# Kernel optimization log

Measured on AMD Instinct MI355X. Metric: run time of the kernel, lower is better.

Reference implementation:

```python
import jax, jax.numpy as jnp
import numpy as np

NUM_HEADS = 1


def setup_inputs() -> dict:
    key = jax.random.key(0)
    k1, k2, k3 = jax.random.split(key, 3)
    B, C, H, W = 32, 1024, 32, 32
    x = jax.random.normal(k1, (B, C, H, W), dtype=jnp.float32)
    w_qkv = jax.random.normal(k2, (3 * C, C), dtype=jnp.float32) * (C ** -0.5)
    w_proj = jax.random.normal(k3, (C, C), dtype=jnp.float32) * (C ** -0.5)
    b_proj = jnp.zeros((C,), dtype=jnp.float32)
    return {"x": x, "w_qkv": w_qkv, "w_proj": w_proj, "b_proj": b_proj}


def reference(x, w_qkv, w_proj, b_proj):
    B, C, H, W = x.shape
    nh = NUM_HEADS
    hd = C // nh
    S = H * W
    # 1x1 conv (no bias) == channel matmul
    qkv = jnp.einsum('bchw,oc->bohw', x, w_qkv)          # [B, 3C, H, W]
    qkv = qkv.reshape(B * nh, 3 * hd, S)
    q, k, v = jnp.split(qkv, 3, axis=1)                   # each [B*nh, hd, S]
    scale = hd ** -0.25
    attn = jax.nn.softmax(
        jnp.einsum('bct,bcs->bts', q * scale, k * scale), axis=-1)  # [B*nh, S, S]
    # faithful to source einsum 'bts,bcs->bts': sums v over channel dim only
    h = attn * jnp.sum(v, axis=1, keepdims=True)          # [B*nh, S, S]
    h = h.reshape(B, nh * S, H, W)                        # requires nh*S == C
    out = jnp.einsum('bchw,oc->bohw', h, w_proj) + b_proj[None, :, None, None]
    return out + x
```

## Files before the change

kernel.cpp:

```cpp
#include <hip/hip_runtime.h>
#include <hip/hip_bf16.h>
#include <stdint.h>


typedef __attribute__((ext_vector_type(8))) short short8;
typedef __attribute__((ext_vector_type(4))) float f32x4;

__device__ __forceinline__ short f2b(float f) {
    __hip_bfloat16 h = __float2bfloat16(f);
    return *reinterpret_cast<short*>(&h);
}
__device__ __forceinline__ float b2f(short s) {
    __hip_bfloat16 h;
    *reinterpret_cast<short*>(&h) = s;
    return __bfloat162float(h);
}

#define GLOAD16(gp, lp) __builtin_amdgcn_global_load_lds(                      \
    (const __attribute__((address_space(1))) unsigned int*)(gp),               \
    (__attribute__((address_space(3))) unsigned int*)(lp), 16, 0, 0)

#define WAITV4 asm volatile("s_waitcnt vmcnt(4)" ::: "memory")
#define WAITV0 asm volatile("s_waitcnt vmcnt(0)" ::: "memory")
#define WAITL0 asm volatile("s_waitcnt lgkmcnt(0)" ::: "memory")
#define BAR()  { asm volatile("" ::: "memory"); __builtin_amdgcn_s_barrier(); \
                 asm volatile("" ::: "memory"); }

__global__ void k_wvsum(const float* __restrict__ wqkv, float* __restrict__ wvsum) {
    int c = blockIdx.x * 256 + threadIdx.x;
    float s = 0.f;
    const float* p = wqkv + (size_t)2048 * 1024 + c;
    for (int o = 0; o < 1024; ++o) s += p[(size_t)o * 1024];
    wvsum[c] = s;
}

__global__ void k_cvt(const float* __restrict__ in, short* __restrict__ out) {
    int i = (blockIdx.x * 256 + threadIdx.x) * 4;
    #pragma unroll
    for (int j = 0; j < 4; ++j) out[i + j] = f2b(in[i + j]);
}

__global__ void k_xpose(const float* __restrict__ x, const float* __restrict__ wvsum,
                        short* __restrict__ xT, float* __restrict__ vsum) {
    __shared__ float tile[32][33];
    __shared__ float ps[8][32];
    int b = blockIdx.z;
    int s0 = blockIdx.x * 32, c0 = blockIdx.y * 32;
    int tx = threadIdx.x, ty = threadIdx.y;
    const float* xb = x + ((size_t)b << 20);
    float p = 0.f;
    #pragma unroll
    for (int i = 0; i < 4; ++i) {
        int cl = ty + i * 8;
        float v = xb[(size_t)(c0 + cl) * 1024 + s0 + tx];
        tile[cl][tx] = v;
        p += v * wvsum[c0 + cl];
    }
    ps[ty][tx] = p;
    __syncthreads();
    short* xTb = xT + ((size_t)b << 20);
    #pragma unroll
    for (int i = 0; i < 4; ++i) {
        int sl = ty + i * 8;
        xTb[(size_t)(s0 + sl) * 1024 + c0 + tx] = f2b(tile[tx][sl]);
    }
    if (ty == 0) {
        float s = 0.f;
        #pragma unroll
        for (int i = 0; i < 8; ++i) s += ps[i][tx];
        atomicAdd(&vsum[b * 1024 + s0 + tx], s);
    }
}

template <int MODE, int TM, int TN>
__global__ __launch_bounds__(512, 2)
void k_gemm(const short* __restrict__ A0, size_t strideA, int lda,
            const short* __restrict__ B0, size_t strideB, int ldb,
            void* __restrict__ O0, size_t strideO, int ldo,
            float* __restrict__ Z,
            const float* __restrict__ vsum,
            const float* __restrict__ bias,
            const float* __restrict__ xres) {
    __shared__ __align__(16) short As[2 * 256 * 64];
    __shared__ __align__(16) short Bs[2 * 256 * 64];

    constexpr int TPB = TM * TN;
    constexpr int CPX = TPB * 4;
    int wg = blockIdx.x;
    int swz = (wg & 7) * CPX + (wg >> 3);
    int z = swz / TPB;
    int rz = swz - z * TPB;
    int m0 = (rz / TN) * 256, n0 = (rz % TN) * 256;

    int tid = threadIdx.x;
    int wid = tid >> 6, l = tid & 63;
    int wm = wid >> 2, wn = wid & 3;
    int lr = l & 15, lg = l >> 4;

    const short* A = A0 + (size_t)z * strideA;
    const short* Bt = B0 + (size_t)z * strideB;

    int srow = wid * 16 + (l >> 3);
    int scol = ((l & 7) ^ (l >> 3)) * 8;
    const short* gA = A + (size_t)(m0 + srow) * lda + scol;
    const short* gB = Bt + (size_t)(n0 + srow) * ldb + scol;
    char* const ldsA = (char*)As;
    char* const ldsB = (char*)Bs;
    int sdst = wid * 2048;

    auto SA = [&](int buf, int h, int t) __attribute__((always_inline)) {
        const short* g = gA + (size_t)(h * 128) * lda + t * 64;
        char* d = ldsA + buf * 32768 + h * 16384 + sdst;
        GLOAD16(g, d);
        GLOAD16(g + (size_t)8 * lda, d + 1024);
    };
    auto SB = [&](int buf, int h, int t) __attribute__((always_inline)) {
        const short* g = gB + (size_t)(h * 128) * ldb + t * 64;
        char* d = ldsB + buf * 32768 + h * 16384 + sdst;
        GLOAD16(g, d);
        GLOAD16(g + (size_t)8 * ldb, d + 1024);
    };

    int cs0 = ((lg) ^ (lr & 7)) * 16;
    int cs1 = ((4 + lg) ^ (lr & 7)) * 16;
    int arow = (wm * 128 + lr) * 128;
    int brow = (wn * 64 + lr) * 128;

    short8 af[8], bf0[4], bf1[4];
    f32x4 acc[8][4] = {};

    auto LDA_ = [&](int buf, int mh) __attribute__((always_inline)) {
        const char* p = ldsA + buf * 32768 + arow + mh * 64 * 128;
        #pragma unroll
        for (int mi = 0; mi < 4; ++mi) {
            af[mi * 2]     = *(const short8*)(p + mi * 2048 + cs0);
            af[mi * 2 + 1] = *(const short8*)(p + mi * 2048 + cs1);
        }
    };
    auto LDB_ = [&](short8* dst, int buf, int nh) __attribute__((always_inline)) {
        const char* p = ldsB + buf * 32768 + brow + nh * 32 * 128;
        #pragma unroll
        for (int ni = 0; ni < 2; ++ni) {
            dst[ni * 2]     = *(const short8*)(p + ni * 2048 + cs0);
            dst[ni * 2 + 1] = *(const short8*)(p + ni * 2048 + cs1);
        }
    };
    auto MMA = [&](int mh, int nh, const short8* bfp) __attribute__((always_inline)) {
        __builtin_amdgcn_s_setprio(1);
        #pragma unroll
        for (int ks = 0; ks < 2; ++ks)
            #pragma unroll
            for (int mi = 0; mi < 4; ++mi)
                #pragma unroll
                for (int ni = 0; ni < 2; ++ni)
                    acc[mh * 4 + mi][nh * 2 + ni] =
                        __builtin_amdgcn_mfma_f32_16x16x32_bf16(
                            af[mi * 2 + ks], bfp[ni * 2 + ks],
                            acc[mh * 4 + mi][nh * 2 + ni], 0, 0, 0);
        __builtin_amdgcn_s_setprio(0);
    };

    SB(0, 0, 0); SB(0, 1, 0); SA(0, 0, 0); SA(0, 1, 0);
    SB(1, 0, 1); SB(1, 1, 1);
    WAITV4;
    BAR();

    for (int j = 0; j < 7; ++j) {
        int t1 = 2 * j + 1, t2 = 2 * j + 2, t3 = 2 * j + 3;
        LDA_(0, 0); LDB_(bf0, 0, 0); SA(1, 0, t1);
        BAR(); WAITL0; MMA(0, 0, bf0); BAR();
        LDB_(bf1, 0, 1); SA(1, 1, t1);
        BAR(); WAITL0; MMA(0, 1, bf1); BAR();
        LDA_(0, 1); SB(0, 0, t2);
        BAR(); WAITL0; MMA(1, 0, bf0); BAR();
        SB(0, 1, t2); WAITV4;
        BAR(); MMA(1, 1, bf1); BAR();
        LDA_(1, 0); LDB_(bf0, 1, 0); SA(0, 0, t2);
        BAR(); WAITL0; MMA(0, 0, bf0); BAR();
        LDB_(bf1, 1, 1); SA(0, 1, t2);
        BAR(); WAITL0; MMA(0, 1, bf1); BAR();
        LDA_(1, 1); SB(1, 0, t3);
        BAR(); WAITL0; MMA(1, 0, bf0); BAR();
        SB(1, 1, t3); WAITV4;
        BAR(); MMA(1, 1, bf1); BAR();
    }
    LDA_(0, 0); LDB_(bf0, 0, 0); SA(1, 0, 15);
    BAR(); WAITL0; MMA(0, 0, bf0); BAR();
    LDB_(bf1, 0, 1); SA(1, 1, 15);
    BAR(); WAITL0; MMA(0, 1, bf1); BAR();
    LDA_(0, 1);
    BAR(); WAITL0; MMA(1, 0, bf0); BAR();
    WAITV0;
    BAR(); MMA(1, 1, bf1); BAR();
    LDA_(1, 0); LDB_(bf0, 1, 0);
    BAR(); WAITL0; MMA(0, 0, bf0); BAR();
    LDB_(bf1, 1, 1);
    BAR(); WAITL0; MMA(0, 1, bf1); BAR();
    LDA_(1, 1);
    BAR(); WAITL0; MMA(1, 0, bf0); BAR();
    MMA(1, 1, bf1);

    int rb = m0 + wm * 128, cb = n0 + wn * 64;
    if (MODE == 0) {
        short* O = (short*)O0 + (size_t)z * strideO;
        #pragma unroll
        for (int mi = 0; mi < 8; ++mi)
            #pragma unroll
            for (int ni = 0; ni < 4; ++ni)
                #pragma unroll
                for (int r = 0; r < 4; ++r)
                    O[(size_t)(rb + mi * 16 + lg * 4 + r) * ldo + cb + ni * 16 + lr] =
                        f2b(acc[mi][ni][r]);
    } else if (MODE == 1) {
        short* O = (short*)O0 + (size_t)z * strideO;
        float* Zb = Z + z * 1024;
        #pragma unroll
        for (int ni = 0; ni < 4; ++ni) {
            float zs = 0.f;
            #pragma unroll
            for (int mi = 0; mi < 8; ++mi)
                #pragma unroll
                for (int r = 0; r < 4; ++r) {
                    float ev = __expf(acc[mi][ni][r] * 0.03125f);
                    O[(size_t)(rb + mi * 16 + lg * 4 + r) * ldo + cb + ni * 16 + lr] = f2b(ev);
                    zs += ev;
                }
            zs += __shfl_xor(zs, 16);
            zs += __shfl_xor(zs, 32);
            if (l < 16) atomicAdd(&Zb[cb + ni * 16 + l], zs);
        }
    } else {
        float* O = (float*)O0 + (size_t)z * strideO;
        const float* xr = xres + (size_t)z * strideO;
        #pragma unroll
        for (int mi = 0; mi < 8; ++mi)
            #pragma unroll
            for (int ni = 0; ni < 4; ++ni)
                #pragma unroll
                for (int r = 0; r < 4; ++r) {
                    int row = rb + mi * 16 + lg * 4 + r;
                    int col = cb + ni * 16 + lr;
                    O[(size_t)row * ldo + col] = acc[mi][ni][r] * vsum[z * 1024 + col] +
                                                 bias[row] + xr[(size_t)row * ldo + col];
                }
    }
}

__global__ void k_invz(float* Z) {
    int i = blockIdx.x * 256 + threadIdx.x;
    Z[i] = 1.0f / Z[i];
}

__global__ void k_scale(short* __restrict__ attnT, const float* __restrict__ invZ) {
    size_t i8 = ((size_t)blockIdx.x * 256 + threadIdx.x) * 8;
    short8 v = *(short8*)&attnT[i8];
    int b = (int)(i8 >> 20);
    int t = (int)(i8 & 1023);
    const float* iz = invZ + b * 1024 + t;
    #pragma unroll
    for (int j = 0; j < 8; ++j) v[j] = f2b(b2f(v[j]) * iz[j]);
    *(short8*)&attnT[i8] = v;
}

extern "C" void kernel_launch(void* const* d_in, const int* in_sizes, int n_in,
                              void* d_out, int out_size, void* d_ws, size_t ws_size,
                              hipStream_t stream) {
    const float* x     = (const float*)d_in[0];
    const float* wqkv  = (const float*)d_in[1];
    const float* wproj = (const float*)d_in[2];
    const float* bproj = (const float*)d_in[3];
    float* out = (float*)d_out;

    char* ws = (char*)d_ws;
    size_t off = 0;
    auto alloc = [&](size_t bytes) {
        void* p = ws + off;
        off += (bytes + 255) & ~(size_t)255;
        return p;
    };
    float* wvsum = (float*)alloc(1024 * 4);
    short* wqk_b = (short*)alloc((size_t)2048 * 1024 * 2);
    short* wp_b  = (short*)alloc((size_t)1024 * 1024 * 2);
    short* xT    = (short*)alloc((size_t)32 * 1024 * 1024 * 2);
    short* qkT   = (short*)alloc((size_t)32 * 1024 * 2048 * 2);
    short* attnT = (short*)alloc((size_t)32 * 1024 * 1024 * 2);
    float* vsum  = (float*)alloc(32 * 1024 * 4);
    float* Zbuf  = (float*)alloc(32 * 1024 * 4);

    hipMemsetAsync(vsum, 0, 32 * 1024 * 4, stream);
    hipMemsetAsync(Zbuf, 0, 32 * 1024 * 4, stream);

    k_wvsum<<<4, 256, 0, stream>>>(wqkv, wvsum);
    k_cvt<<<2048, 256, 0, stream>>>(wqkv, wqk_b);
    k_cvt<<<1024, 256, 0, stream>>>(wproj, wp_b);
    k_xpose<<<dim3(32, 32, 32), dim3(32, 8), 0, stream>>>(x, wvsum, xT, vsum);

    k_gemm<0, 4, 8><<<1024, 512, 0, stream>>>(
        xT, (size_t)1048576, 1024, wqk_b, 0, 1024,
        qkT, (size_t)2097152, 2048, nullptr, nullptr, nullptr, nullptr);

    k_gemm<1, 4, 4><<<512, 512, 0, stream>>>(
        qkT + 1024, (size_t)2097152, 2048, qkT, (size_t)2097152, 2048,
        attnT, (size_t)1048576, 1024, Zbuf, nullptr, nullptr, nullptr);

    k_invz<<<128, 256, 0, stream>>>(Zbuf);
    k_scale<<<16384, 256, 0, stream>>>(attnT, Zbuf);

    k_gemm<2, 4, 4><<<512, 512, 0, stream>>>(
        wp_b, 0, 1024, attnT, (size_t)1048576, 1024,
        out, (size_t)1048576, 1024, nullptr, vsum, bproj, x);
}
```

Measured before the change: 448.5 us.

## Restructure GEMM main loop to prefetch LDS fragments one phase ahead

Replaces the unrolled 8-phase GEMM schedule with a compact 16-iteration loop that uses separate A fragment registers for each M half. The next tile's first A and B fragments are read from LDS before the final MMA of the current tile, and the explicit lgkmcnt(0) waits are removed so LDS reads can overlap MFMA work. This is meant to hide LDS read latency behind matrix math. It raises register pressure and relies on compiler-inserted waits and the barriers for correctness. The vsum parameter is also renamed to scale.

Result: slower. 485.5 us (+8.3%).

```diff
diff --git a/kernel.cpp b/kernel.cpp
--- a/kernel.cpp
+++ b/kernel.cpp
@@ -22,7 +22,6 @@
 
 #define WAITV4 asm volatile("s_waitcnt vmcnt(4)" ::: "memory")
 #define WAITV0 asm volatile("s_waitcnt vmcnt(0)" ::: "memory")
-#define WAITL0 asm volatile("s_waitcnt lgkmcnt(0)" ::: "memory")
 #define BAR()  { asm volatile("" ::: "memory"); __builtin_amdgcn_s_barrier(); \
                  asm volatile("" ::: "memory"); }
 
@@ -78,7 +77,7 @@
             const short* __restrict__ B0, size_t strideB, int ldb,
             void* __restrict__ O0, size_t strideO, int ldo,
             float* __restrict__ Z,
-            const float* __restrict__ vsum,
+            const float* __restrict__ scale,
             const float* __restrict__ bias,
             const float* __restrict__ xres) {
     __shared__ __align__(16) short As[2 * 256 * 64];
@@ -126,26 +125,27 @@
     int arow = (wm * 128 + lr) * 128;
     int brow = (wn * 64 + lr) * 128;
 
-    short8 af[8], bf0[4], bf1[4];
+    short8 afA[8], afB[8], bfc[4], bfa[4];
     f32x4 acc[8][4] = {};
 
-    auto LDA_ = [&](int buf, int mh) __attribute__((always_inline)) {
-        const char* p = ldsA + buf * 32768 + arow + mh * 64 * 128;
+    auto RDA = [&](short8* dst, int buf, int mh) __attribute__((always_inline)) {
+        const char* p = ldsA + buf * 32768 + arow + mh * 8192;
         #pragma unroll
         for (int mi = 0; mi < 4; ++mi) {
-            af[mi * 2]     = *(const short8*)(p + mi * 2048 + cs0);
-            af[mi * 2 + 1] = *(const short8*)(p + mi * 2048 + cs1);
+            dst[mi * 2]     = *(const short8*)(p + mi * 2048 + cs0);
+            dst[mi * 2 + 1] = *(const short8*)(p + mi * 2048 + cs1);
         }
     };
-    auto LDB_ = [&](short8* dst, int buf, int nh) __attribute__((always_inline)) {
-        const char* p = ldsB + buf * 32768 + brow + nh * 32 * 128;
+    auto RDB = [&](short8* dst, int buf, int nh) __attribute__((always_inline)) {
+        const char* p = ldsB + buf * 32768 + brow + nh * 4096;
         #pragma unroll
         for (int ni = 0; ni < 2; ++ni) {
             dst[ni * 2]     = *(const short8*)(p + ni * 2048 + cs0);
             dst[ni * 2 + 1] = *(const short8*)(p + ni * 2048 + cs1);
         }
     };
-    auto MMA = [&](int mh, int nh, const short8* bfp) __attribute__((always_inline)) {
+    auto MMA = [&](const short8* afp, const short8* bfp, int mh, int nh)
+        __attribute__((always_inline)) {
         __builtin_amdgcn_s_setprio(1);
         #pragma unroll
         for (int ks = 0; ks < 2; ++ks)
@@ -155,7 +155,7 @@
                 for (int ni = 0; ni < 2; ++ni)
                     acc[mh * 4 + mi][nh * 2 + ni] =
                         __builtin_amdgcn_mfma_f32_16x16x32_bf16(
-                            af[mi * 2 + ks], bfp[ni * 2 + ks],
+                            afp[mi * 2 + ks], bfp[ni * 2 + ks],
                             acc[mh * 4 + mi][nh * 2 + ni], 0, 0, 0);
         __builtin_amdgcn_s_setprio(0);
     };
@@ -164,41 +164,25 @@
     SB(1, 0, 1); SB(1, 1, 1);
     WAITV4;
     BAR();
-
-    for (int j = 0; j < 7; ++j) {
-        int t1 = 2 * j + 1, t2 = 2 * j + 2, t3 = 2 * j + 3;
-        LDA_(0, 0); LDB_(bf0, 0, 0); SA(1, 0, t1);
-        BAR(); WAITL0; MMA(0, 0, bf0); BAR();
-        LDB_(bf1, 0, 1); SA(1, 1, t1);
-        BAR(); WAITL0; MMA(0, 1, bf1); BAR();
-        LDA_(0, 1); SB(0, 0, t2);
-        BAR(); WAITL0; MMA(1, 0, bf0); BAR();
-        SB(0, 1, t2); WAITV4;
-        BAR(); MMA(1, 1, bf1); BAR();
-        LDA_(1, 0); LDB_(bf0, 1, 0); SA(0, 0, t2);
-        BAR(); WAITL0; MMA(0, 0, bf0); BAR();
-        LDB_(bf1, 1, 1); SA(0, 1, t2);
-        BAR(); WAITL0; MMA(0, 1, bf1); BAR();
-        LDA_(1, 1); SB(1, 0, t3);
-        BAR(); WAITL0; MMA(1, 0, bf0); BAR();
-        SB(1, 1, t3); WAITV4;
-        BAR(); MMA(1, 1, bf1); BAR();
-    }
-    LDA_(0, 0); LDB_(bf0, 0, 0); SA(1, 0, 15);
-    BAR(); WAITL0; MMA(0, 0, bf0); BAR();
-    LDB_(bf1, 0, 1); SA(1, 1, 15);
-    BAR(); WAITL0; MMA(0, 1, bf1); BAR();
-    LDA_(0, 1);
-    BAR(); WAITL0; MMA(1, 0, bf0); BAR();
-    WAITV0;
-    BAR(); MMA(1, 1, bf1); BAR();
-    LDA_(1, 0); LDB_(bf0, 1, 0);
-    BAR(); WAITL0; MMA(0, 0, bf0); BAR();
-    LDB_(bf1, 1, 1);
-    BAR(); WAITL0; MMA(0, 1, bf1); BAR();
-    LDA_(1, 1);
-    BAR(); WAITL0; MMA(1, 0, bf0); BAR();
-    MMA(1, 1, bf1);
+    RDA(afA, 0, 0); RDB(bfc, 0, 0);
+
+    for (int t = 0; t < 16; ++t) {
+        int b = t & 1;
+        RDB(bfa, b, 1);
+        if (t < 15) SA(b ^ 1, 0, t + 1);
+        BAR(); MMA(afA, bfc, 0, 0); BAR();
+        RDA(afB, b, 1);
+        if (t < 15) SA(b ^ 1, 1, t + 1);
+        BAR(); MMA(afA, bfa, 0, 1); BAR();
+        if (t < 14) SB(b, 0, t + 2);
+        BAR(); MMA(afB, bfc, 1, 0); BAR();
+        if (t < 14) SB(b, 1, t + 2);
+        if (t <= 13) { WAITV4; } else if (t == 14) { WAITV0; }
+        BAR();
+        if (t < 15) { RDA(afA, b ^ 1, 0); RDB(bfc, b ^ 1, 0); }
+        MMA(afB, bfa, 1, 1);
+        BAR();
+    }
 
     int rb = m0 + wm * 128, cb = n0 + wn * 64;
     if (MODE == 0) {
@@ -240,7 +224,7 @@
                 for (int r = 0; r < 4; ++r) {
                     int row = rb + mi * 16 + lg * 4 + r;
                     int col = cb + ni * 16 + lr;
-                    O[(size_t)row * ldo + col] = acc[mi][ni][r] * vsum[z * 1024 + col] +
+                    O[(size_t)row * ldo + col] = acc[mi][ni][r] * scale[z * 1024 + col] +
                                                  bias[row] + xr[(size_t)row * ldo + col];
                 }
     }
```
